# Kernel tuning notes

Measured on AMD Instinct MI355X. Metric: run time of the kernel, lower is better.

The kernel has to match this reference:

```python
import jax, jax.numpy as jnp
import numpy as np


def _maxpool3d(x, win):
    # x: (B, C, D, H, W); SAME padding via w//2 on each spatial side, stride 1
    pads = [(0, 0), (0, 0)] + [(w // 2, w // 2) for w in win]
    return jax.lax.reduce_window(x, -jnp.inf, jax.lax.max,
                                 (1, 1) + tuple(win), (1, 1, 1, 1, 1), pads)


def _soft_skeletonize(x, thresh_width=5):
    # Iterative morphological erosion: x <- relu(x - relu(maxpool(minpool(x)) - minpool(x)))
    for _ in range(thresh_width):
        p1 = -_maxpool3d(-x, (3, 1, 1))  # directional min-pool along D
        p2 = -_maxpool3d(-x, (1, 3, 1))  # along H
        p3 = -_maxpool3d(-x, (1, 1, 3))  # along W
        min_pool = jnp.minimum(jnp.minimum(p1, p2), p3)
        contour = jax.nn.relu(_maxpool3d(min_pool, (3, 3, 3)) - min_pool)
        x = jax.nn.relu(x - contour)
    return x


def _positive_intersection(center_line, vessel):
    B, C = center_line.shape[0], center_line.shape[1]
    clf = center_line.reshape(B, C, -1)
    vf = vessel.reshape(B, C, -1)
    intersection = jnp.sum(clf * vf, axis=-1).sum(0)          # (C,)
    return (intersection + 1e-12) / (jnp.sum(clf, axis=-1).sum(0) + 1e-12)


def setup_inputs() -> dict:
    key = jax.random.key(0)
    k1, k2 = jax.random.split(key)
    B, C, D, H, W = 2, 1, 64, 256, 256
    logits = jax.random.normal(k1, (B, C, D, H, W), dtype=jnp.float32)
    target = jax.random.uniform(k2, (B, C, D, H, W), dtype=jnp.float32)
    mask = jnp.ones((B, C, D, H, W), dtype=jnp.float32)
    return {"logits": logits, "target": target, "mask": mask}


def reference(logits, target, mask):
    THRESH_WIDTH = 5
    pred = jax.nn.sigmoid(logits) * mask
    tgt = target * mask
    target_skeleton = _soft_skeletonize(tgt, THRESH_WIDTH)
    cl_pred = _soft_skeletonize(pred, THRESH_WIDTH)
    clrecall = _positive_intersection(target_skeleton, pred)[0]
    clacc = _positive_intersection(cl_pred, tgt)[0]
    cldice = 2.0 * clrecall * clacc / (clrecall + clacc + 1e-12)
    return 1.0 - cldice
```

## Files before the change

kernel.cpp:

```cpp
#include <hip/hip_runtime.h>
#include <math.h>


constexpr int Bn = 2;
constexpr int D  = 64;
constexpr int H  = 256;
constexpr int W  = 256;
constexpr int HW = H * W;
constexpr int NV = Bn * D * H * W;

constexpr int CD  = 16;
constexpr int XSF = 76;
constexpr int RSF = 68;

__device__ __forceinline__ float4 vmin4(float4 a, float4 b) {
    return make_float4(fminf(a.x,b.x), fminf(a.y,b.y), fminf(a.z,b.z), fminf(a.w,b.w));
}
__device__ __forceinline__ float4 vmax4(float4 a, float4 b) {
    return make_float4(fmaxf(a.x,b.x), fmaxf(a.y,b.y), fmaxf(a.z,b.z), fmaxf(a.w,b.w));
}
__device__ __forceinline__ float4 sh1(float4 a, float4 b) { return make_float4(a.y,a.z,a.w,b.x); }
__device__ __forceinline__ float4 sh3(float4 a, float4 b) { return make_float4(a.w,b.x,b.y,b.z); }

__global__ __launch_bounds__(256) void prep_kernel(const float* __restrict__ logits,
                                                   const float* __restrict__ target,
                                                   const float* __restrict__ mask,
                                                   float* __restrict__ pred,
                                                   float* __restrict__ tgt) {
    int i = (blockIdx.x * 256 + threadIdx.x) * 4;
    float4 lg = *(const float4*)(logits + i);
    float4 tg = *(const float4*)(target + i);
    float4 mk = *(const float4*)(mask + i);
    float4 p, t;
    p.x = (1.0f/(1.0f+expf(-lg.x)))*mk.x;  t.x = tg.x*mk.x;
    p.y = (1.0f/(1.0f+expf(-lg.y)))*mk.y;  t.y = tg.y*mk.y;
    p.z = (1.0f/(1.0f+expf(-lg.z)))*mk.z;  t.z = tg.z*mk.z;
    p.w = (1.0f/(1.0f+expf(-lg.w)))*mk.w;  t.w = tg.w*mk.w;
    *(float4*)(pred + i) = p;
    *(float4*)(tgt + i)  = t;
}

template <bool FINAL>
__global__ __launch_bounds__(256) void skel_iter_kernel(
        const float* __restrict__ in0, float* __restrict__ out0,
        const float* __restrict__ oth0, double* __restrict__ acc0,
        const float* __restrict__ in1, float* __restrict__ out1,
        const float* __restrict__ oth1, double* __restrict__ acc1) {
    __shared__ float sx[4][36 * XSF];
    __shared__ float srm[2][34 * RSF];

    int cpx = gridDim.x >> 3;
    int hwb = blockIdx.x;
    int bx  = (hwb & 7) * cpx + (hwb >> 3);

    int t   = bx >> 8;
    int bt  = bx & 255;
    int w0  = (bt & 3) * 64;
    int h0  = ((bt >> 2) & 7) * 32;
    int gd0 = ((bt >> 5) & 3) * CD;
    int b   = (bt >> 7) & 1;

    const float* xin  = t ? in1  : in0;
    float*       xout = t ? out1 : out0;
    const float* oth  = t ? oth1 : oth0;
    double*      accp = t ? acc1 : acc0;

    int tid = threadIdx.x;
    int r   = tid >> 3;
    int k   = tid & 7;

    const float* xb  = xin + b * (D * HW);
    float*       ob  = xout ? (xout + b * (D * HW)) : nullptr;
    const float* otb = oth + b * (D * HW);

    const float4 INF4  = make_float4( INFINITY,  INFINITY,  INFINITY,  INFINITY);
    const float4 NINF4 = make_float4(-INFINITY, -INFINITY, -INFINITY, -INFINITY);

    int j1 = tid + 256, j2 = tid + 512;
    int sr0 = tid / 18, sq0 = tid - sr0 * 18;
    int sr1 = j1 / 18,  sq1 = j1 - sr1 * 18;
    int sr2 = j2 / 18,  sq2 = j2 - sr2 * 18;
    bool has2 = (j2 < 648);

    float4 Pa, Pb, Pc;
    auto issue = [&](int p) {
        if (p < 0 || p >= D) { Pa = Pb = Pc = INF4; return; }
        const float* pl = xb + p * HW;
        auto f = [&](int row, int qd) -> float4 {
            int gh = h0 - 2 + row;
            int gw = w0 - 4 + 4 * qd;
            if ((unsigned)gh < (unsigned)H && (unsigned)gw < (unsigned)W)
                return *(const float4*)(pl + gh * W + gw);
            return INF4;
        };
        Pa = f(sr0, sq0);
        Pb = f(sr1, sq1);
        Pc = has2 ? f(sr2, sq2) : INF4;
    };
    auto commitv = [&](int p, float4 va, float4 vb, float4 vc) {
        float* dst = sx[(p + 4) & 3];
        *(float4*)&dst[sr0 * XSF + 4 * sq0] = va;
        *(float4*)&dst[sr1 * XSF + 4 * sq1] = vb;
        if (has2) *(float4*)&dst[sr2 * XSF + 4 * sq2] = vc;
    };

    issue(gd0 - 2); commitv(gd0 - 2, Pa, Pb, Pc);
    issue(gd0 - 1); commitv(gd0 - 1, Pa, Pb, Pc);
    issue(gd0);     commitv(gd0,     Pa, Pb, Pc);
    issue(gd0 + 1);
    __syncthreads();

    float4 h1lo=NINF4, h1hi=NINF4, h2lo=NINF4, h2hi=NINF4;
    float4 p1lo=NINF4, p1hi=NINF4, p2lo=NINF4, p2hi=NINF4;
    float4 rmplo=NINF4, rmphi=NINF4;
    float4 xplo=INF4, xphi=INF4;
    double s0 = 0.0, s1 = 0.0;

    for (int s = gd0 - 1; s <= gd0 + CD + 1; ++s) {
        float4 Ta = Pa, Tb = Pb, Tc = Pc;
        if (s + 3 <= gd0 + CD + 1) issue(s + 3);
        if (s + 2 <= gd0 + CD + 1) commitv(s + 2, Ta, Tb, Tc);

        bool sv = (s >= 0 && s < D && s <= gd0 + CD);
        float4 lo = NINF4, hi = NINF4, rmlo = NINF4, rmhi = NINF4;
        if (sv) {
            const float* xq = sx[(s + 4) & 3];
            const float* xm = sx[(s + 3) & 3];
            const float* xp = sx[(s + 5) & 3];
            {
                const float* rc  = &xq[(r + 2) * XSF + 8 * k];
                const float* ru  = &xq[(r + 1) * XSF + 8 * k];
                const float* rd  = &xq[(r + 3) * XSF + 8 * k];
                const float* rm_ = &xm[(r + 2) * XSF + 8 * k];
                const float* rp_ = &xp[(r + 2) * XSF + 8 * k];
                float4 X0 = *(const float4*)rc,        X1 = *(const float4*)(rc + 4),
                       X2 = *(const float4*)(rc + 8),  X3 = *(const float4*)(rc + 12);
                float4 U1 = *(const float4*)(ru + 4),  U2 = *(const float4*)(ru + 8);
                float4 Dn1= *(const float4*)(rd + 4),  Dn2= *(const float4*)(rd + 8);
                float4 M1 = *(const float4*)(rm_ + 4), M2 = *(const float4*)(rm_ + 8);
                float4 P1 = *(const float4*)(rp_ + 4), P2 = *(const float4*)(rp_ + 8);
                lo = vmin4(vmin4(sh3(X0, X1), X1), sh1(X1, X2));
                lo = vmin4(lo, vmin4(vmin4(U1, Dn1), vmin4(M1, P1)));
                hi = vmin4(vmin4(sh3(X1, X2), X2), sh1(X2, X3));
                hi = vmin4(hi, vmin4(vmin4(U2, Dn2), vmin4(M2, P2)));
                float eL = __shfl_up(hi.w, 1);
                float eR = __shfl_down(lo.x, 1);
                if (k == 0) {
                    eL = -INFINITY;
                    if (w0 > 0) {
                        float w3 = fminf(fminf(X0.z, X0.w), X1.x);
                        eL = fminf(fminf(w3, fminf(ru[3], rd[3])),
                                   fminf(rm_[3], rp_[3]));
                    }
                }
                if (k == 7) {
                    eR = -INFINITY;
                    if (w0 + 64 < W) {
                        float w3 = fminf(fminf(X2.w, X3.x), X3.y);
                        eR = fminf(fminf(w3, fminf(ru[12], rd[12])),
                                   fminf(rm_[12], rp_[12]));
                    }
                }
                rmlo = vmax4(vmax4(make_float4(eL, lo.x, lo.y, lo.z), lo),
                             make_float4(lo.y, lo.z, lo.w, hi.x));
                rmhi = vmax4(vmax4(make_float4(lo.w, hi.x, hi.y, hi.z), hi),
                             make_float4(hi.y, hi.z, hi.w, eR));
                float* rw = &srm[s & 1][(r + 1) * RSF + 8 * k];
                *(float4*)rw       = rmlo;
                *(float4*)(rw + 4) = rmhi;
            }
            if (tid < 16) {
                int mr2 = (tid >> 3) ? 33 : 0;
                int k2  = tid & 7;
                int gh2 = h0 - 1 + mr2;
                float4 hlo = NINF4, hhi = NINF4;
                if ((unsigned)gh2 < (unsigned)H) {
                    int xr2 = mr2 + 1;
                    const float* rc  = &xq[xr2 * XSF + 8 * k2];
                    const float* ru  = &xq[(xr2 - 1) * XSF + 8 * k2];
                    const float* rd  = &xq[(xr2 + 1) * XSF + 8 * k2];
                    const float* rm_ = &xm[xr2 * XSF + 8 * k2];
                    const float* rp_ = &xp[xr2 * XSF + 8 * k2];
                    float4 X0 = *(const float4*)rc,        X1 = *(const float4*)(rc + 4),
                           X2 = *(const float4*)(rc + 8),  X3 = *(const float4*)(rc + 12);
                    float4 U1 = *(const float4*)(ru + 4),  U2 = *(const float4*)(ru + 8);
                    float4 Dn1= *(const float4*)(rd + 4),  Dn2= *(const float4*)(rd + 8);
                    float4 M1 = *(const float4*)(rm_ + 4), M2 = *(const float4*)(rm_ + 8);
                    float4 P1 = *(const float4*)(rp_ + 4), P2 = *(const float4*)(rp_ + 8);
                    float4 l2 = vmin4(vmin4(sh3(X0, X1), X1), sh1(X1, X2));
                    l2 = vmin4(l2, vmin4(vmin4(U1, Dn1), vmin4(M1, P1)));
                    float4 g2 = vmin4(vmin4(sh3(X1, X2), X2), sh1(X2, X3));
                    g2 = vmin4(g2, vmin4(vmin4(U2, Dn2), vmin4(M2, P2)));
                    float eL2 = -INFINITY, eR2 = -INFINITY;
                    if (w0 + 8 * k2 - 1 >= 0) {
                        float w3 = fminf(fminf(X0.z, X0.w), X1.x);
                        eL2 = fminf(fminf(w3, fminf(ru[3], rd[3])),
                                    fminf(rm_[3], rp_[3]));
                    }
                    if (w0 + 8 * k2 + 8 < W) {
                        float w3 = fminf(fminf(X2.w, X3.x), X3.y);
                        eR2 = fminf(fminf(w3, fminf(ru[12], rd[12])),
                                    fminf(rm_[12], rp_[12]));
                    }
                    hlo = vmax4(vmax4(make_float4(eL2, l2.x, l2.y, l2.z), l2),
                                make_float4(l2.y, l2.z, l2.w, g2.x));
                    hhi = vmax4(vmax4(make_float4(l2.w, g2.x, g2.y, g2.z), g2),
                                make_float4(g2.y, g2.z, g2.w, eR2));
                }
                float* hw = &srm[s & 1][mr2 * RSF + 8 * k2];
                *(float4*)hw       = hlo;
                *(float4*)(hw + 4) = hhi;
            }
        }

        int dm = s - 1;
        float4 xclo = INF4, xchi = INF4;
        if (dm >= gd0 && dm <= gd0 + CD - 1) {
            const float* xd = sx[(dm + 4) & 3];
            xclo = *(const float4*)&xd[(r + 2) * XSF + 8 * k + 4];
            xchi = *(const float4*)&xd[(r + 2) * XSF + 8 * k + 8];
        }

        float4 hclo = NINF4, hchi = NINF4;
        if (s >= gd0 && dm >= 0 && dm < D) {
            const float* m = srm[dm & 1];
            float4 a0 = *(const float4*)&m[r * RSF + 8 * k];
            float4 a1 = *(const float4*)&m[r * RSF + 8 * k + 4];
            float4 b0 = *(const float4*)&m[(r + 2) * RSF + 8 * k];
            float4 b1 = *(const float4*)&m[(r + 2) * RSF + 8 * k + 4];
            hclo = vmax4(vmax4(a0, rmplo), b0);
            hchi = vmax4(vmax4(a1, rmphi), b1);
        }

        int d = s - 2;
        if (d >= gd0 && d <= gd0 + CD - 1) {
            float4 mxlo = vmax4(h2lo, vmax4(h1lo, hclo));
            float4 mxhi = vmax4(h2hi, vmax4(h1hi, hchi));
            float4 rlo, rhi;
            rlo.x = fmaxf(xplo.x - (mxlo.x - p2lo.x), 0.0f);
            rlo.y = fmaxf(xplo.y - (mxlo.y - p2lo.y), 0.0f);
            rlo.z = fmaxf(xplo.z - (mxlo.z - p2lo.z), 0.0f);
            rlo.w = fmaxf(xplo.w - (mxlo.w - p2lo.w), 0.0f);
            rhi.x = fmaxf(xphi.x - (mxhi.x - p2hi.x), 0.0f);
            rhi.y = fmaxf(xphi.y - (mxhi.y - p2hi.y), 0.0f);
            rhi.z = fmaxf(xphi.z - (mxhi.z - p2hi.z), 0.0f);
            rhi.w = fmaxf(xphi.w - (mxhi.w - p2hi.w), 0.0f);
            long off = (long)d * HW + (h0 + r) * W + (w0 + 8 * k);
            if constexpr (FINAL) {
                float4 o1 = *(const float4*)(otb + off);
                float4 o2 = *(const float4*)(otb + off + 4);
                s0 += (double)(rlo.x * o1.x) + (double)(rlo.y * o1.y)
                    + (double)(rlo.z * o1.z) + (double)(rlo.w * o1.w)
                    + (double)(rhi.x * o2.x) + (double)(rhi.y * o2.y)
                    + (double)(rhi.z * o2.z) + (double)(rhi.w * o2.w);
                s1 += (double)rlo.x + (double)rlo.y + (double)rlo.z + (double)rlo.w
                    + (double)rhi.x + (double)rhi.y + (double)rhi.z + (double)rhi.w;
            } else {
                *(float4*)(ob + off)     = rlo;
                *(float4*)(ob + off + 4) = rhi;
            }
        }

        h2lo = h1lo; h2hi = h1hi; h1lo = hclo; h1hi = hchi;
        p2lo = p1lo; p2hi = p1hi; p1lo = lo;   p1hi = hi;
        rmplo = rmlo; rmphi = rmhi;
        xplo = xclo;  xphi = xchi;

        __syncthreads();
    }

    if constexpr (FINAL) {
        for (int off = 32; off > 0; off >>= 1) {
            s0 += __shfl_down(s0, off, 64);
            s1 += __shfl_down(s1, off, 64);
        }
        if ((tid & 63) == 0) {
            atomicAdd(&accp[0], s0);
            atomicAdd(&accp[1], s1);
        }
    }
}

__global__ void final_kernel(const double* __restrict__ acc, float* __restrict__ out) {
    double clrecall = (acc[0] + 1e-12) / (acc[1] + 1e-12);
    double clacc    = (acc[2] + 1e-12) / (acc[3] + 1e-12);
    double cldice   = 2.0 * clrecall * clacc / (clrecall + clacc + 1e-12);
    out[0] = (float)(1.0 - cldice);
}

extern "C" void kernel_launch(void* const* d_in, const int* in_sizes, int n_in,
                              void* d_out, int out_size, void* d_ws, size_t ws_size,
                              hipStream_t stream) {
    const float* logits = (const float*)d_in[0];
    const float* target = (const float*)d_in[1];
    const float* mask   = (const float*)d_in[2];
    float* out = (float*)d_out;

    float* pred = (float*)d_ws;
    float* tgt  = pred + NV;
    float* A0   = tgt + NV;
    float* B0   = A0 + NV;

    bool big = ws_size >= (size_t)6 * NV * 4 + 64;
    float* A1   = big ? (B0 + NV) : A0;
    float* B1   = big ? (A1 + NV) : B0;
    double* acc = big ? (double*)(B1 + NV) : (double*)(B0 + NV);

    hipMemsetAsync(acc, 0, 4 * sizeof(double), stream);

    dim3 blk(256);
    prep_kernel<<<dim3(NV / 1024), blk, 0, stream>>>(logits, target, mask, pred, tgt);

    if (big) {
        dim3 g(512);
        skel_iter_kernel<false><<<g, blk, 0, stream>>>(tgt, A0, pred, acc, pred, A1, tgt, acc + 2);
        skel_iter_kernel<false><<<g, blk, 0, stream>>>(A0, B0, pred, acc, A1, B1, tgt, acc + 2);
        skel_iter_kernel<false><<<g, blk, 0, stream>>>(B0, A0, pred, acc, B1, A1, tgt, acc + 2);
        skel_iter_kernel<false><<<g, blk, 0, stream>>>(A0, B0, pred, acc, A1, B1, tgt, acc + 2);
        skel_iter_kernel<true ><<<g, blk, 0, stream>>>(B0, nullptr, pred, acc, B1, nullptr, tgt, acc + 2);
    } else {
        dim3 g(256);
        skel_iter_kernel<false><<<g, blk, 0, stream>>>(tgt, A0, pred, acc, tgt, A0, pred, acc);
        skel_iter_kernel<false><<<g, blk, 0, stream>>>(A0, B0, pred, acc, A0, B0, pred, acc);
        skel_iter_kernel<false><<<g, blk, 0, stream>>>(B0, A0, pred, acc, B0, A0, pred, acc);
        skel_iter_kernel<false><<<g, blk, 0, stream>>>(A0, B0, pred, acc, A0, B0, pred, acc);
        skel_iter_kernel<true ><<<g, blk, 0, stream>>>(B0, nullptr, pred, acc, B0, nullptr, pred, acc);
        skel_iter_kernel<false><<<g, blk, 0, stream>>>(pred, A0, tgt, acc + 2, pred, A0, tgt, acc + 2);
        skel_iter_kernel<false><<<g, blk, 0, stream>>>(A0, B0, tgt, acc + 2, A0, B0, tgt, acc + 2);
        skel_iter_kernel<false><<<g, blk, 0, stream>>>(B0, A0, tgt, acc + 2, B0, A0, tgt, acc + 2);
        skel_iter_kernel<false><<<g, blk, 0, stream>>>(A0, B0, tgt, acc + 2, A0, B0, tgt, acc + 2);
        skel_iter_kernel<true ><<<g, blk, 0, stream>>>(B0, nullptr, tgt, acc + 2, B0, nullptr, tgt, acc + 2);
    }

    final_kernel<<<1, 1, 0, stream>>>(acc, out);
}
```

Measured before the change: 331.0 us.

## Halve depth chunk, double grid, and compute row max in-step with extra barrier

The depth chunk per block shrinks from 16 to 8 slices and the grid doubles, so more blocks cover the GPU's compute units. The H-direction max of the row-max buffer is now computed in the same step as its write, using a single srm buffer and an extra __syncthreads, rather than one step later from a double buffer. This shortens the register pipeline by a stage and trims one loop iteration. In exchange there is more halo reloading per output slice, since the two-slice halo is amortised over fewer slices, plus an additional barrier in every iteration.

```diff
diff --git a/kernel.cpp b/kernel.cpp
--- a/kernel.cpp
+++ b/kernel.cpp
@@ -9,7 +9,7 @@
 constexpr int HW = H * W;
 constexpr int NV = Bn * D * H * W;
 
-constexpr int CD  = 16;
+constexpr int CD  = 8;
 constexpr int XSF = 76;
 constexpr int RSF = 68;
 
@@ -47,18 +47,18 @@
         const float* __restrict__ in1, float* __restrict__ out1,
         const float* __restrict__ oth1, double* __restrict__ acc1) {
     __shared__ float sx[4][36 * XSF];
-    __shared__ float srm[2][34 * RSF];
+    __shared__ float srm[34 * RSF];
 
     int cpx = gridDim.x >> 3;
     int hwb = blockIdx.x;
     int bx  = (hwb & 7) * cpx + (hwb >> 3);
 
-    int t   = bx >> 8;
-    int bt  = bx & 255;
+    int t   = bx >> 9;
+    int bt  = bx & 511;
     int w0  = (bt & 3) * 64;
     int h0  = ((bt >> 2) & 7) * 32;
-    int gd0 = ((bt >> 5) & 3) * CD;
-    int b   = (bt >> 7) & 1;
+    int gd0 = ((bt >> 5) & 7) * CD;
+    int b   = (bt >> 8) & 1;
 
     const float* xin  = t ? in1  : in0;
     float*       xout = t ? out1 : out0;
@@ -111,17 +111,15 @@
     __syncthreads();
 
     float4 h1lo=NINF4, h1hi=NINF4, h2lo=NINF4, h2hi=NINF4;
-    float4 p1lo=NINF4, p1hi=NINF4, p2lo=NINF4, p2hi=NINF4;
-    float4 rmplo=NINF4, rmphi=NINF4;
-    float4 xplo=INF4, xphi=INF4;
+    float4 p1lo=NINF4, p1hi=NINF4;
     double s0 = 0.0, s1 = 0.0;
 
-    for (int s = gd0 - 1; s <= gd0 + CD + 1; ++s) {
+    for (int s = gd0 - 1; s <= gd0 + CD; ++s) {
         float4 Ta = Pa, Tb = Pb, Tc = Pc;
         if (s + 3 <= gd0 + CD + 1) issue(s + 3);
         if (s + 2 <= gd0 + CD + 1) commitv(s + 2, Ta, Tb, Tc);
 
-        bool sv = (s >= 0 && s < D && s <= gd0 + CD);
+        bool sv = (s >= 0 && s < D);
         float4 lo = NINF4, hi = NINF4, rmlo = NINF4, rmhi = NINF4;
         if (sv) {
             const float* xq = sx[(s + 4) & 3];
@@ -165,7 +163,7 @@
                              make_float4(lo.y, lo.z, lo.w, hi.x));
                 rmhi = vmax4(vmax4(make_float4(lo.w, hi.x, hi.y, hi.z), hi),
                              make_float4(hi.y, hi.z, hi.w, eR));
-                float* rw = &srm[s & 1][(r + 1) * RSF + 8 * k];
+                float* rw = &srm[(r + 1) * RSF + 8 * k];
                 *(float4*)rw       = rmlo;
                 *(float4*)(rw + 4) = rmhi;
             }
@@ -207,44 +205,45 @@
                     hhi = vmax4(vmax4(make_float4(l2.w, g2.x, g2.y, g2.z), g2),
                                 make_float4(g2.y, g2.z, g2.w, eR2));
                 }
-                float* hw = &srm[s & 1][mr2 * RSF + 8 * k2];
+                float* hw = &srm[mr2 * RSF + 8 * k2];
                 *(float4*)hw       = hlo;
                 *(float4*)(hw + 4) = hhi;
             }
         }
 
-        int dm = s - 1;
+        int d = s - 1;
+        bool dv = (d >= gd0 && d <= gd0 + CD - 1);
         float4 xclo = INF4, xchi = INF4;
-        if (dm >= gd0 && dm <= gd0 + CD - 1) {
-            const float* xd = sx[(dm + 4) & 3];
+        if (dv) {
+            const float* xd = sx[(s + 3) & 3];
             xclo = *(const float4*)&xd[(r + 2) * XSF + 8 * k + 4];
             xchi = *(const float4*)&xd[(r + 2) * XSF + 8 * k + 8];
         }
 
+        __syncthreads();
+
         float4 hclo = NINF4, hchi = NINF4;
-        if (s >= gd0 && dm >= 0 && dm < D) {
-            const float* m = srm[dm & 1];
-            float4 a0 = *(const float4*)&m[r * RSF + 8 * k];
-            float4 a1 = *(const float4*)&m[r * RSF + 8 * k + 4];
-            float4 b0 = *(const float4*)&m[(r + 2) * RSF + 8 * k];
-            float4 b1 = *(const float4*)&m[(r + 2) * RSF + 8 * k + 4];
-            hclo = vmax4(vmax4(a0, rmplo), b0);
-            hchi = vmax4(vmax4(a1, rmphi), b1);
-        }
-
-        int d = s - 2;
-        if (d >= gd0 && d <= gd0 + CD - 1) {
+        if (sv) {
+            float4 a0 = *(const float4*)&srm[r * RSF + 8 * k];
+            float4 a1 = *(const float4*)&srm[r * RSF + 8 * k + 4];
+            float4 b0 = *(const float4*)&srm[(r + 2) * RSF + 8 * k];
+            float4 b1 = *(const float4*)&srm[(r + 2) * RSF + 8 * k + 4];
+            hclo = vmax4(vmax4(a0, rmlo), b0);
+            hchi = vmax4(vmax4(a1, rmhi), b1);
+        }
+
+        if (dv) {
             float4 mxlo = vmax4(h2lo, vmax4(h1lo, hclo));
             float4 mxhi = vmax4(h2hi, vmax4(h1hi, hchi));
             float4 rlo, rhi;
-            rlo.x = fmaxf(xplo.x - (mxlo.x - p2lo.x), 0.0f);
-            rlo.y = fmaxf(xplo.y - (mxlo.y - p2lo.y), 0.0f);
-            rlo.z = fmaxf(xplo.z - (mxlo.z - p2lo.z), 0.0f);
-            rlo.w = fmaxf(xplo.w - (mxlo.w - p2lo.w), 0.0f);
-            rhi.x = fmaxf(xphi.x - (mxhi.x - p2hi.x), 0.0f);
-            rhi.y = fmaxf(xphi.y - (mxhi.y - p2hi.y), 0.0f);
-            rhi.z = fmaxf(xphi.z - (mxhi.z - p2hi.z), 0.0f);
-            rhi.w = fmaxf(xphi.w - (mxhi.w - p2hi.w), 0.0f);
+            rlo.x = fmaxf(xclo.x - (mxlo.x - p1lo.x), 0.0f);
+            rlo.y = fmaxf(xclo.y - (mxlo.y - p1lo.y), 0.0f);
+            rlo.z = fmaxf(xclo.z - (mxlo.z - p1lo.z), 0.0f);
+            rlo.w = fmaxf(xclo.w - (mxlo.w - p1lo.w), 0.0f);
+            rhi.x = fmaxf(xchi.x - (mxhi.x - p1hi.x), 0.0f);
+            rhi.y = fmaxf(xchi.y - (mxhi.y - p1hi.y), 0.0f);
+            rhi.z = fmaxf(xchi.z - (mxhi.z - p1hi.z), 0.0f);
+            rhi.w = fmaxf(xchi.w - (mxhi.w - p1hi.w), 0.0f);
             long off = (long)d * HW + (h0 + r) * W + (w0 + 8 * k);
             if constexpr (FINAL) {
                 float4 o1 = *(const float4*)(otb + off);
@@ -262,9 +261,7 @@
         }
 
         h2lo = h1lo; h2hi = h1hi; h1lo = hclo; h1hi = hchi;
-        p2lo = p1lo; p2hi = p1hi; p1lo = lo;   p1hi = hi;
-        rmplo = rmlo; rmphi = rmhi;
-        xplo = xclo;  xphi = xchi;
+        p1lo = lo;   p1hi = hi;
 
         __syncthreads();
     }
@@ -312,14 +309,14 @@
     prep_kernel<<<dim3(NV / 1024), blk, 0, stream>>>(logits, target, mask, pred, tgt);
 
     if (big) {
-        dim3 g(512);
+        dim3 g(1024);
         skel_iter_kernel<false><<<g, blk, 0, stream>>>(tgt, A0, pred, acc, pred, A1, tgt, acc + 2);
         skel_iter_kernel<false><<<g, blk, 0, stream>>>(A0, B0, pred, acc, A1, B1, tgt, acc + 2);
         skel_iter_kernel<false><<<g, blk, 0, stream>>>(B0, A0, pred, acc, B1, A1, tgt, acc + 2);
         skel_iter_kernel<false><<<g, blk, 0, stream>>>(A0, B0, pred, acc, A1, B1, tgt, acc + 2);
         skel_iter_kernel<true ><<<g, blk, 0, stream>>>(B0, nullptr, pred, acc, B1, nullptr, tgt, acc + 2);
     } else {
-        dim3 g(256);
+        dim3 g(512);
         skel_iter_kernel<false><<<g, blk, 0, stream>>>(tgt, A0, pred, acc, tgt, A0, pred, acc);
         skel_iter_kernel<false><<<g, blk, 0, stream>>>(A0, B0, pred, acc, A0, B0, pred, acc);
         skel_iter_kernel<false><<<g, blk, 0, stream>>>(B0, A0, pred, acc, B0, A0, pred, acc);
```

New measurement: 412.0 us. 24.5% more time.

## Split depth into 6 uneven chunks, keep previous slice in registers, 3-slot LDS ring

Applied to the files above, without the earlier changes.

Changes the depth decomposition from 4 chunks of 16 to 6 chunks of about 10-11 slices, raising the grid from 512 to 768 blocks for better CU coverage on the device. The previous depth slice's centre values are now carried in registers rather than reread from a fourth shared-memory buffer, so the LDS ring shrinks from 4 to 3 slots, which lowers LDS use and may allow more resident blocks. The halo-row cross-min logic is factored into a shared helper. In exchange, more halo slices are reloaded per chunk, and the modulo-3 indexing plus extra live registers add overhead.

```diff
diff --git a/kernel.cpp b/kernel.cpp
--- a/kernel.cpp
+++ b/kernel.cpp
@@ -9,7 +9,6 @@
 constexpr int HW = H * W;
 constexpr int NV = Bn * D * H * W;
 
-constexpr int CD  = 16;
 constexpr int XSF = 76;
 constexpr int RSF = 68;
 
@@ -46,19 +45,23 @@
         const float* __restrict__ oth0, double* __restrict__ acc0,
         const float* __restrict__ in1, float* __restrict__ out1,
         const float* __restrict__ oth1, double* __restrict__ acc1) {
-    __shared__ float sx[4][36 * XSF];
+    __shared__ float sx[3][36 * XSF];
     __shared__ float srm[2][34 * RSF];
 
     int cpx = gridDim.x >> 3;
     int hwb = blockIdx.x;
     int bx  = (hwb & 7) * cpx + (hwb >> 3);
 
-    int t   = bx >> 8;
-    int bt  = bx & 255;
-    int w0  = (bt & 3) * 64;
-    int h0  = ((bt >> 2) & 7) * 32;
-    int gd0 = ((bt >> 5) & 3) * CD;
-    int b   = (bt >> 7) & 1;
+    int t   = (bx >= 384) ? 1 : 0;
+    int bt  = bx - 384 * t;
+    int ti  = bt & 31;
+    int w0  = (ti & 3) * 64;
+    int h0  = (ti >> 2) * 32;
+    int cc  = bt >> 5;
+    int b   = (cc >= 6) ? 1 : 0;
+    int c   = cc - 6 * b;
+    int gs  = (32 * c) / 3;
+    int CDc = (32 * (c + 1)) / 3 - gs;
 
     const float* xin  = t ? in1  : in0;
     float*       xout = t ? out1 : out0;
@@ -98,131 +101,130 @@
         Pc = has2 ? f(sr2, sq2) : INF4;
     };
     auto commitv = [&](int p, float4 va, float4 vb, float4 vc) {
-        float* dst = sx[(p + 4) & 3];
+        float* dst = sx[(p + 6) % 3];
         *(float4*)&dst[sr0 * XSF + 4 * sq0] = va;
         *(float4*)&dst[sr1 * XSF + 4 * sq1] = vb;
         if (has2) *(float4*)&dst[sr2 * XSF + 4 * sq2] = vc;
     };
 
-    issue(gd0 - 2); commitv(gd0 - 2, Pa, Pb, Pc);
-    issue(gd0 - 1); commitv(gd0 - 1, Pa, Pb, Pc);
-    issue(gd0);     commitv(gd0,     Pa, Pb, Pc);
-    issue(gd0 + 1);
+    auto crossrm = [&](const float* xq, const float* xp, int xrow, int kk,
+                       bool rowOK, bool leftOK, bool rightOK,
+                       float4 cM1, float4 cM2, float cx0w, float cx3x,
+                       float4& lo, float4& hi, float4& rmlo, float4& rmhi,
+                       float4& oX1, float4& oX2, float& ox0w, float& ox3x) {
+        const float* rc = &xq[xrow * XSF + 8 * kk];
+        const float* ru = rc - XSF;
+        const float* rd = rc + XSF;
+        const float* rp = &xp[xrow * XSF + 8 * kk];
+        float4 X0 = *(const float4*)rc,       X1 = *(const float4*)(rc + 4),
+               X2 = *(const float4*)(rc + 8), X3 = *(const float4*)(rc + 12);
+        float4 U1 = *(const float4*)(ru + 4), U2 = *(const float4*)(ru + 8);
+        float4 D1 = *(const float4*)(rd + 4), D2 = *(const float4*)(rd + 8);
+        float4 P1 = *(const float4*)(rp + 4), P2 = *(const float4*)(rp + 8);
+        oX1 = X1; oX2 = X2; ox0w = X0.w; ox3x = X3.x;
+        lo = vmin4(vmin4(sh3(X0, X1), X1), sh1(X1, X2));
+        lo = vmin4(lo, vmin4(vmin4(U1, D1), vmin4(cM1, P1)));
+        hi = vmin4(vmin4(sh3(X1, X2), X2), sh1(X2, X3));
+        hi = vmin4(hi, vmin4(vmin4(U2, D2), vmin4(cM2, P2)));
+        float eL = __shfl_up(hi.w, 1);
+        float eR = __shfl_down(lo.x, 1);
+        if (kk == 0) {
+            eL = -INFINITY;
+            if (leftOK) {
+                float w3 = fminf(fminf(X0.z, X0.w), X1.x);
+                eL = fminf(fminf(w3, fminf(ru[3], rd[3])), fminf(cx0w, rp[3]));
+            }
+        }
+        if (kk == 7) {
+            eR = -INFINITY;
+            if (rightOK) {
+                float w3 = fminf(fminf(X2.w, X3.x), X3.y);
+                eR = fminf(fminf(w3, fminf(ru[12], rd[12])), fminf(cx3x, rp[12]));
+            }
+        }
+        if (!rowOK) { lo = NINF4; hi = NINF4; eL = -INFINITY; eR = -INFINITY; }
+        rmlo = vmax4(vmax4(make_float4(eL, lo.x, lo.y, lo.z), lo),
+                     make_float4(lo.y, lo.z, lo.w, hi.x));
+        rmhi = vmax4(vmax4(make_float4(lo.w, hi.x, hi.y, hi.z), hi),
+                     make_float4(hi.y, hi.z, hi.w, eR));
+    };
+
+    float4 cM1 = INF4, cM2 = INF4;  float cx0w = INFINITY, cx3x = INFINITY;
+    float4 hM1 = INF4, hM2 = INF4;  float hx0w = INFINITY, hx3x = INFINITY;
+    {
+        int p = gs - 2;
+        if (p >= 0) {
+            const float* pl = xb + p * HW;
+            auto q = [&](int gh, int gw) -> float4 {
+                if ((unsigned)gh < (unsigned)H && (unsigned)gw < (unsigned)W)
+                    return *(const float4*)(pl + gh * W + gw);
+                return INF4;
+            };
+            int gh = h0 + r;
+            int gw = w0 - 4 + 8 * k;
+            float4 X0 = q(gh, gw), X1 = q(gh, gw + 4),
+                   X2 = q(gh, gw + 8), X3 = q(gh, gw + 12);
+            cM1 = X1; cM2 = X2; cx0w = X0.w; cx3x = X3.x;
+            if (tid < 16) {
+                int mr2 = (tid >> 3) ? 33 : 0;
+                int k2  = tid & 7;
+                int gh2 = h0 - 2 + (mr2 + 1);
+                int gw2 = w0 - 4 + 8 * k2;
+                float4 Y0 = q(gh2, gw2), Y1 = q(gh2, gw2 + 4),
+                       Y2 = q(gh2, gw2 + 8), Y3 = q(gh2, gw2 + 12);
+                hM1 = Y1; hM2 = Y2; hx0w = Y0.w; hx3x = Y3.x;
+            }
+        }
+    }
+
+    issue(gs - 1); commitv(gs - 1, Pa, Pb, Pc);
+    issue(gs);     commitv(gs,     Pa, Pb, Pc);
+    issue(gs + 1);
     __syncthreads();
 
     float4 h1lo=NINF4, h1hi=NINF4, h2lo=NINF4, h2hi=NINF4;
     float4 p1lo=NINF4, p1hi=NINF4, p2lo=NINF4, p2hi=NINF4;
     float4 rmplo=NINF4, rmphi=NINF4;
-    float4 xplo=INF4, xphi=INF4;
+    float4 XC1=INF4, XC2=INF4;
     double s0 = 0.0, s1 = 0.0;
 
-    for (int s = gd0 - 1; s <= gd0 + CD + 1; ++s) {
+    for (int s = gs - 1; s <= gs + CDc + 1; ++s) {
         float4 Ta = Pa, Tb = Pb, Tc = Pc;
-        if (s + 3 <= gd0 + CD + 1) issue(s + 3);
-        if (s + 2 <= gd0 + CD + 1) commitv(s + 2, Ta, Tb, Tc);
-
-        bool sv = (s >= 0 && s < D && s <= gd0 + CD);
+        if (s + 3 <= gs + CDc + 1) issue(s + 3);
+        if (s + 2 <= gs + CDc + 1) commitv(s + 2, Ta, Tb, Tc);
+
+        bool sv = (s >= 0 && s < D && s <= gs + CDc);
         float4 lo = NINF4, hi = NINF4, rmlo = NINF4, rmhi = NINF4;
+        float4 nM1 = INF4, nM2 = INF4;  float nx0w = INFINITY, nx3x = INFINITY;
+        float4 nH1 = INF4, nH2 = INF4;  float nhx0w = INFINITY, nhx3x = INFINITY;
         if (sv) {
-            const float* xq = sx[(s + 4) & 3];
-            const float* xm = sx[(s + 3) & 3];
-            const float* xp = sx[(s + 5) & 3];
-            {
-                const float* rc  = &xq[(r + 2) * XSF + 8 * k];
-                const float* ru  = &xq[(r + 1) * XSF + 8 * k];
-                const float* rd  = &xq[(r + 3) * XSF + 8 * k];
-                const float* rm_ = &xm[(r + 2) * XSF + 8 * k];
-                const float* rp_ = &xp[(r + 2) * XSF + 8 * k];
-                float4 X0 = *(const float4*)rc,        X1 = *(const float4*)(rc + 4),
-                       X2 = *(const float4*)(rc + 8),  X3 = *(const float4*)(rc + 12);
-                float4 U1 = *(const float4*)(ru + 4),  U2 = *(const float4*)(ru + 8);
-                float4 Dn1= *(const float4*)(rd + 4),  Dn2= *(const float4*)(rd + 8);
-                float4 M1 = *(const float4*)(rm_ + 4), M2 = *(const float4*)(rm_ + 8);
-                float4 P1 = *(const float4*)(rp_ + 4), P2 = *(const float4*)(rp_ + 8);
-                lo = vmin4(vmin4(sh3(X0, X1), X1), sh1(X1, X2));
-                lo = vmin4(lo, vmin4(vmin4(U1, Dn1), vmin4(M1, P1)));
-                hi = vmin4(vmin4(sh3(X1, X2), X2), sh1(X2, X3));
-                hi = vmin4(hi, vmin4(vmin4(U2, Dn2), vmin4(M2, P2)));
-                float eL = __shfl_up(hi.w, 1);
-                float eR = __shfl_down(lo.x, 1);
-                if (k == 0) {
-                    eL = -INFINITY;
-                    if (w0 > 0) {
-                        float w3 = fminf(fminf(X0.z, X0.w), X1.x);
-                        eL = fminf(fminf(w3, fminf(ru[3], rd[3])),
-                                   fminf(rm_[3], rp_[3]));
-                    }
-                }
-                if (k == 7) {
-                    eR = -INFINITY;
-                    if (w0 + 64 < W) {
-                        float w3 = fminf(fminf(X2.w, X3.x), X3.y);
-                        eR = fminf(fminf(w3, fminf(ru[12], rd[12])),
-                                   fminf(rm_[12], rp_[12]));
-                    }
-                }
-                rmlo = vmax4(vmax4(make_float4(eL, lo.x, lo.y, lo.z), lo),
-                             make_float4(lo.y, lo.z, lo.w, hi.x));
-                rmhi = vmax4(vmax4(make_float4(lo.w, hi.x, hi.y, hi.z), hi),
-                             make_float4(hi.y, hi.z, hi.w, eR));
-                float* rw = &srm[s & 1][(r + 1) * RSF + 8 * k];
-                *(float4*)rw       = rmlo;
-                *(float4*)(rw + 4) = rmhi;
-            }
+            const float* xq = sx[(s + 6) % 3];
+            const float* xp = sx[(s + 7) % 3];
+            crossrm(xq, xp, r + 2, k, true,
+                    (w0 + 8 * k) > 0, (w0 + 8 * k + 8) < W,
+                    cM1, cM2, cx0w, cx3x,
+                    lo, hi, rmlo, rmhi, nM1, nM2, nx0w, nx3x);
+            float* rw = &srm[s & 1][(r + 1) * RSF + 8 * k];
+            *(float4*)rw       = rmlo;
+            *(float4*)(rw + 4) = rmhi;
             if (tid < 16) {
                 int mr2 = (tid >> 3) ? 33 : 0;
                 int k2  = tid & 7;
-                int gh2 = h0 - 1 + mr2;
-                float4 hlo = NINF4, hhi = NINF4;
-                if ((unsigned)gh2 < (unsigned)H) {
-                    int xr2 = mr2 + 1;
-                    const float* rc  = &xq[xr2 * XSF + 8 * k2];
-                    const float* ru  = &xq[(xr2 - 1) * XSF + 8 * k2];
-                    const float* rd  = &xq[(xr2 + 1) * XSF + 8 * k2];
-                    const float* rm_ = &xm[xr2 * XSF + 8 * k2];
-                    const float* rp_ = &xp[xr2 * XSF + 8 * k2];
-                    float4 X0 = *(const float4*)rc,        X1 = *(const float4*)(rc + 4),
-                           X2 = *(const float4*)(rc + 8),  X3 = *(const float4*)(rc + 12);
-                    float4 U1 = *(const float4*)(ru + 4),  U2 = *(const float4*)(ru + 8);
-                    float4 Dn1= *(const float4*)(rd + 4),  Dn2= *(const float4*)(rd + 8);
-                    float4 M1 = *(const float4*)(rm_ + 4), M2 = *(const float4*)(rm_ + 8);
-                    float4 P1 = *(const float4*)(rp_ + 4), P2 = *(const float4*)(rp_ + 8);
-                    float4 l2 = vmin4(vmin4(sh3(X0, X1), X1), sh1(X1, X2));
-                    l2 = vmin4(l2, vmin4(vmin4(U1, Dn1), vmin4(M1, P1)));
-                    float4 g2 = vmin4(vmin4(sh3(X1, X2), X2), sh1(X2, X3));
-                    g2 = vmin4(g2, vmin4(vmin4(U2, Dn2), vmin4(M2, P2)));
-                    float eL2 = -INFINITY, eR2 = -INFINITY;
-                    if (w0 + 8 * k2 - 1 >= 0) {
-                        float w3 = fminf(fminf(X0.z, X0.w), X1.x);
-                        eL2 = fminf(fminf(w3, fminf(ru[3], rd[3])),
-                                    fminf(rm_[3], rp_[3]));
-                    }
-                    if (w0 + 8 * k2 + 8 < W) {
-                        float w3 = fminf(fminf(X2.w, X3.x), X3.y);
-                        eR2 = fminf(fminf(w3, fminf(ru[12], rd[12])),
-                                    fminf(rm_[12], rp_[12]));
-                    }
-                    hlo = vmax4(vmax4(make_float4(eL2, l2.x, l2.y, l2.z), l2),
-                                make_float4(l2.y, l2.z, l2.w, g2.x));
-                    hhi = vmax4(vmax4(make_float4(l2.w, g2.x, g2.y, g2.z), g2),
-                                make_float4(g2.y, g2.z, g2.w, eR2));
-                }
+                bool rowOK = (mr2 == 0) ? (h0 > 0) : (h0 + 32 < H);
+                float4 qlo, qhi, qrmlo, qrmhi;
+                crossrm(xq, xp, mr2 + 1, k2, rowOK,
+                        (w0 + 8 * k2) > 0, (w0 + 8 * k2 + 8) < W,
+                        hM1, hM2, hx0w, hx3x,
+                        qlo, qhi, qrmlo, qrmhi, nH1, nH2, nhx0w, nhx3x);
                 float* hw = &srm[s & 1][mr2 * RSF + 8 * k2];
-                *(float4*)hw       = hlo;
-                *(float4*)(hw + 4) = hhi;
+                *(float4*)hw       = qrmlo;
+                *(float4*)(hw + 4) = qrmhi;
             }
         }
 
         int dm = s - 1;
-        float4 xclo = INF4, xchi = INF4;
-        if (dm >= gd0 && dm <= gd0 + CD - 1) {
-            const float* xd = sx[(dm + 4) & 3];
-            xclo = *(const float4*)&xd[(r + 2) * XSF + 8 * k + 4];
-            xchi = *(const float4*)&xd[(r + 2) * XSF + 8 * k + 8];
-        }
-
         float4 hclo = NINF4, hchi = NINF4;
-        if (s >= gd0 && dm >= 0 && dm < D) {
+        if (s >= gs && dm >= 0 && dm < D) {
             const float* m = srm[dm & 1];
             float4 a0 = *(const float4*)&m[r * RSF + 8 * k];
             float4 a1 = *(const float4*)&m[r * RSF + 8 * k + 4];
@@ -233,18 +235,18 @@
         }
 
         int d = s - 2;
-        if (d >= gd0 && d <= gd0 + CD - 1) {
+        if (d >= gs && d <= gs + CDc - 1) {
             float4 mxlo = vmax4(h2lo, vmax4(h1lo, hclo));
             float4 mxhi = vmax4(h2hi, vmax4(h1hi, hchi));
             float4 rlo, rhi;
-            rlo.x = fmaxf(xplo.x - (mxlo.x - p2lo.x), 0.0f);
-            rlo.y = fmaxf(xplo.y - (mxlo.y - p2lo.y), 0.0f);
-            rlo.z = fmaxf(xplo.z - (mxlo.z - p2lo.z), 0.0f);
-            rlo.w = fmaxf(xplo.w - (mxlo.w - p2lo.w), 0.0f);
-            rhi.x = fmaxf(xphi.x - (mxhi.x - p2hi.x), 0.0f);
-            rhi.y = fmaxf(xphi.y - (mxhi.y - p2hi.y), 0.0f);
-            rhi.z = fmaxf(xphi.z - (mxhi.z - p2hi.z), 0.0f);
-            rhi.w = fmaxf(xphi.w - (mxhi.w - p2hi.w), 0.0f);
+            rlo.x = fmaxf(XC1.x - (mxlo.x - p2lo.x), 0.0f);
+            rlo.y = fmaxf(XC1.y - (mxlo.y - p2lo.y), 0.0f);
+            rlo.z = fmaxf(XC1.z - (mxlo.z - p2lo.z), 0.0f);
+            rlo.w = fmaxf(XC1.w - (mxlo.w - p2lo.w), 0.0f);
+            rhi.x = fmaxf(XC2.x - (mxhi.x - p2hi.x), 0.0f);
+            rhi.y = fmaxf(XC2.y - (mxhi.y - p2hi.y), 0.0f);
+            rhi.z = fmaxf(XC2.z - (mxhi.z - p2hi.z), 0.0f);
+            rhi.w = fmaxf(XC2.w - (mxhi.w - p2hi.w), 0.0f);
             long off = (long)d * HW + (h0 + r) * W + (w0 + 8 * k);
             if constexpr (FINAL) {
                 float4 o1 = *(const float4*)(otb + off);
@@ -264,7 +266,9 @@
         h2lo = h1lo; h2hi = h1hi; h1lo = hclo; h1hi = hchi;
         p2lo = p1lo; p2hi = p1hi; p1lo = lo;   p1hi = hi;
         rmplo = rmlo; rmphi = rmhi;
-        xplo = xclo;  xphi = xchi;
+        XC1 = cM1; XC2 = cM2;
+        cM1 = nM1; cM2 = nM2; cx0w = nx0w; cx3x = nx3x;
+        hM1 = nH1; hM2 = nH2; hx0w = nhx0w; hx3x = nhx3x;
 
         __syncthreads();
     }
@@ -312,14 +316,14 @@
     prep_kernel<<<dim3(NV / 1024), blk, 0, stream>>>(logits, target, mask, pred, tgt);
 
     if (big) {
-        dim3 g(512);
+        dim3 g(768);
         skel_iter_kernel<false><<<g, blk, 0, stream>>>(tgt, A0, pred, acc, pred, A1, tgt, acc + 2);
         skel_iter_kernel<false><<<g, blk, 0, stream>>>(A0, B0, pred, acc, A1, B1, tgt, acc + 2);
         skel_iter_kernel<false><<<g, blk, 0, stream>>>(B0, A0, pred, acc, B1, A1, tgt, acc + 2);
         skel_iter_kernel<false><<<g, blk, 0, stream>>>(A0, B0, pred, acc, A1, B1, tgt, acc + 2);
         skel_iter_kernel<true ><<<g, blk, 0, stream>>>(B0, nullptr, pred, acc, B1, nullptr, tgt, acc + 2);
     } else {
-        dim3 g(256);
+        dim3 g(384);
         skel_iter_kernel<false><<<g, blk, 0, stream>>>(tgt, A0, pred, acc, tgt, A0, pred, acc);
         skel_iter_kernel<false><<<g, blk, 0, stream>>>(A0, B0, pred, acc, A0, B0, pred, acc);
         skel_iter_kernel<false><<<g, blk, 0, stream>>>(B0, A0, pred, acc, B0, A0, pred, acc);
```

After: 361.9 us. 1.09x slower.
